# Performance work log

Hardware: AMD Instinct MI355X
Metric: run time of the kernel (lower is better)

The kernel has to match this reference:

```python
import jax, jax.numpy as jnp
import numpy as np

IC = 64   # inter_channels
S = 3     # num_subset_S
ST = 2    # num_subset_T


def _bn(x, g, b):
    # BatchNorm2d in eval mode with running_mean=0, running_var=1, eps=1e-5
    return x * (g / jnp.sqrt(1.0 + 1e-5))[:, None, None] + b[:, None, None]


def _c1(x, W, b):
    # 1x1 Conv2d over (N, C, T, V)
    return jnp.einsum('oc,nctv->notv', W, x) + b[None, :, None, None]


def setup_inputs() -> dict:
    key = jax.random.key(0)
    ks = iter(jax.random.split(key, 40))
    r = lambda sh: jax.random.normal(next(ks), sh, dtype=jnp.float32) * 0.05
    N, C, T, V = 64, 128, 64, 25
    d = {}
    d['x'] = jax.random.normal(next(ks), (N, C, T, V), dtype=jnp.float32)
    d['W_ins'] = r((2 * S * IC, C)); d['b_ins'] = r((2 * S * IC,))
    d['alphas'] = jnp.ones((1, S, 1, 1), jnp.float32)
    d['att0s'] = jnp.full((1, S, V, V), 1.0 / V, jnp.float32)
    d['W_outs'] = r((C, S * C)); d['b_outs'] = r((C,))
    d['g_outs'] = jnp.ones((C,), jnp.float32) + r((C,)); d['be_outs'] = r((C,))
    d['W_ffs'] = r((C, C)); d['b_ffs'] = r((C,))
    d['g_ffs'] = jnp.ones((C,), jnp.float32) + r((C,)); d['be_ffs'] = r((C,))
    d['W_int'] = r((4 * ST * IC, C)); d['b_int'] = r((4 * ST * IC,))
    d['alphat_b'] = jnp.ones((1, ST, 1, 1), jnp.float32)
    d['alphat_f'] = jnp.ones((1, ST, 1, 1), jnp.float32)
    d['W_outt'] = r((C, 2 * ST * C)); d['b_outt'] = r((C,))
    d['g_outt'] = jnp.ones((C,), jnp.float32) + r((C,)); d['be_outt'] = r((C,))
    d['W_fft'] = r((C, C)); d['b_fft'] = r((C,))
    d['g_fft'] = jnp.ones((C,), jnp.float32) + r((C,)); d['be_fft'] = r((C,))
    d['W_tcn'] = r((C, C, 7, 1)); d['b_tcn'] = r((C,))
    d['g_tcn'] = jnp.ones((C,), jnp.float32) + r((C,)); d['be_tcn'] = r((C,))
    return d


def reference(x, W_ins, b_ins, alphas, att0s, W_outs, b_outs, g_outs, be_outs,
              W_ffs, b_ffs, g_ffs, be_ffs, W_int, b_int, alphat_b, alphat_f,
              W_outt, b_outt, g_outt, be_outt, W_fft, b_fft, g_fft, be_fft,
              W_tcn, b_tcn, g_tcn, be_tcn):
    N, C, T, V = x.shape
    lrelu = lambda a: jax.nn.leaky_relu(a, 0.1)

    # ---- spatial attention ----
    qk = _c1(x, W_ins, b_ins).reshape(N, 2 * S, IC, T, V)
    q, k = qk[:, :S], qk[:, S:]
    att = jnp.tanh(jnp.einsum('nsctu,nsctv->nsuv', q, k) / (IC * T)) * alphas + att0s
    y = jnp.einsum('nctu,nsuv->nsctv', x, att).reshape(N, S * C, T, V)
    y = lrelu(x + _bn(_c1(y, W_outs, b_outs), g_outs, be_outs))   # out_nets + residual
    y = lrelu(x + _bn(_c1(y, W_ffs, b_ffs), g_ffs, be_ffs))       # ff_nets + residual (downs2 = identity)

    # ---- directed temporal attention ----
    bm = jnp.triu(jnp.ones((T, T), x.dtype))  # backward mask
    fm = bm.T                                  # forward mask (tril)
    qk = _c1(y, W_int, b_int).reshape(N, 4 * ST, IC, T, V)
    q_f, q_b = qk[:, :ST], qk[:, ST:2 * ST]
    k_f, k_b = qk[:, 2 * ST:3 * ST], qk[:, 3 * ST:]
    att_b = jnp.tanh(jnp.einsum('nsctv,nscqv->nstq', q_b, k_b) / (IC * V)) * alphat_b * bm
    att_f = jnp.tanh(jnp.einsum('nsctv,nscqv->nstq', q_f, k_f) / (IC * V)) * alphat_f * fm
    z_f = jnp.einsum('nctv,nstq->nscqv', y, att_f).reshape(N, ST * C, T, V)
    z_b = jnp.einsum('nctv,nstq->nscqv', y, att_b).reshape(N, ST * C, T, V)
    z = jnp.concatenate([z_f, z_b], axis=1)                        # (N, 2*ST*C, T, V)
    z = lrelu(y + _bn(_c1(z, W_outt, b_outt), g_outt, be_outt))    # out_nett + residual
    z = lrelu(y + _bn(_c1(z, W_fft, b_fft), g_fft, be_fft))        # ff_nett + residual

    # ---- TCN extension: (7,1) temporal conv + BN + residual ----
    z1 = jax.lax.conv_general_dilated(z, W_tcn, (1, 1), ((3, 3), (0, 0)),
                                      dimension_numbers=('NCHW', 'OIHW', 'NCHW'))
    z1 = _bn(z1 + b_tcn[None, :, None, None] - b_tcn[None, :, None, None] + b_tcn[None, :, None, None], g_tcn, be_tcn) if False else _bn(z1 + b_tcn[None, :, None, None], g_tcn, be_tcn)
    z = lrelu(z + z1)
    return z
```

## Files before the change

### kernel.cpp

```cpp
#include <hip/hip_runtime.h>

#define BNSC 0.99999500003749963f

typedef _Float16 f16;
typedef _Float16 f16x8 __attribute__((ext_vector_type(8)));
typedef float    f32x4 __attribute__((ext_vector_type(4)));

static __device__ __forceinline__ float lrelu_f(float a) { return a >= 0.0f ? a : 0.1f * a; }

static __device__ __forceinline__ void xcd_swz(int& bx, int& by, int& bz) {
    const int GX = gridDim.x, GY = gridDim.y, GZ = gridDim.z;
    if (((GX * GZ) & 7) == 0) {
        const int lin = blockIdx.x + GX * (blockIdx.y + GY * blockIdx.z);
        const int xcd = lin & 7;
        const int rest = lin >> 3;
        by = rest % GY;
        const int g = (rest / GY) * 8 + xcd;
        bx = g % GX;
        bz = g / GX;
    } else {
        bx = blockIdx.x; by = blockIdx.y; bz = blockIdx.z;
    }
}

__global__ __launch_bounds__(256) void prep_w_k(
    const float* __restrict__ Wins, const float* __restrict__ Wouts,
    const float* __restrict__ Wffs, const float* __restrict__ Wint,
    const float* __restrict__ Woutt, const float* __restrict__ Wfft,
    const float* __restrict__ Wtcn, f16* __restrict__ dst)
{
    int i = blockIdx.x * 256 + threadIdx.x;
    int o = 0;
    if (i < 49152) { dst[o + i] = (f16)Wins[i];  return; } i -= 49152; o += 49152;
    if (i < 49152) { dst[o + i] = (f16)Wouts[i]; return; } i -= 49152; o += 49152;
    if (i < 16384) { dst[o + i] = (f16)Wffs[i];  return; } i -= 16384; o += 16384;
    if (i < 65536) { dst[o + i] = (f16)Wint[i];  return; } i -= 65536; o += 65536;
    if (i < 65536) { dst[o + i] = (f16)Woutt[i]; return; } i -= 65536; o += 65536;
    if (i < 16384) { dst[o + i] = (f16)Wfft[i];  return; } i -= 16384; o += 16384;
    if (i < 114688) {
        int tau = i / 16384, rem = i - tau * 16384;
        dst[o + i] = (f16)Wtcn[(size_t)rem * 7 + tau];
    }
}

__global__ __launch_bounds__(256) void x_to_T_k(const float* __restrict__ x,
                                                f16* __restrict__ xT, f16* __restrict__ xBp)
{
    __shared__ float L[64 * 68];
    const int n = blockIdx.z, tv0 = blockIdx.x * 64, c0 = blockIdx.y * 64;
    const int tid = threadIdx.x;
    const int cc = tid >> 4, tv4 = (tid & 15) * 4;
    f16* xBn = xBp + (size_t)n * 262144;
    #pragma unroll
    for (int p = 0; p < 4; ++p) {
        const int c = cc + p * 16;
        float4 v = *(const float4*)&x[((size_t)n * 128 + c0 + c) * 1600 + tv0 + tv4];
        *(float4*)&L[c * 68 + tv4] = v;
        const float vv[4] = {v.x, v.y, v.z, v.w};
        #pragma unroll
        for (int e = 0; e < 4; ++e) {
            const int tvg = tv0 + tv4 + e;
            const int t = tvg / 25, u = tvg - t * 25;
            xBn[(size_t)(c0 + c) * 2048 + t * 32 + u] = (f16)vv[e];
        }
    }
    __syncthreads();
    const int tv = tid & 63, cb = (tid >> 6) * 16;
    f16x8 o0, o1;
    #pragma unroll
    for (int i = 0; i < 8; ++i) o0[i] = (f16)L[(cb + i) * 68 + tv];
    #pragma unroll
    for (int i = 0; i < 8; ++i) o1[i] = (f16)L[(cb + 8 + i) * 68 + tv];
    f16* dst = &xT[((size_t)n * 1600 + tv0 + tv) * 128 + c0 + cb];
    *(f16x8*)dst = o0;
    *(f16x8*)(dst + 8) = o1;
}

__global__ __launch_bounds__(256) void T_to_out_k(const f16* __restrict__ oT, float* __restrict__ out)
{
    __shared__ float L[128 * 69];
    const int n = blockIdx.z, tv0 = blockIdx.x * 64;
    const int tid = threadIdx.x;
    #pragma unroll
    for (int p = 0; p < 4; ++p) {
        int idx = tid + p * 256;
        int tv = idx >> 4, c8 = (idx & 15) * 8;
        f16x8 v = *(const f16x8*)&oT[((size_t)n * 1600 + tv0 + tv) * 128 + c8];
        #pragma unroll
        for (int i = 0; i < 8; ++i) L[(c8 + i) * 69 + tv] = (float)v[i];
    }
    __syncthreads();
    const int c = tid >> 1, tvb = (tid & 1) * 32;
    #pragma unroll
    for (int j = 0; j < 8; ++j) {
        float4 o;
        o.x = L[c * 69 + tvb + j * 4 + 0];
        o.y = L[c * 69 + tvb + j * 4 + 1];
        o.z = L[c * 69 + tvb + j * 4 + 2];
        o.w = L[c * 69 + tvb + j * 4 + 3];
        *(float4*)&out[((size_t)n * 128 + c) * 1600 + tv0 + tvb + j * 4] = o;
    }
}

template<int EPI>
__global__ __launch_bounds__(256) void gemm_t_k(
    const f16* __restrict__ A, const f16* __restrict__ W,
    const float* __restrict__ bias,
    const float* __restrict__ g, const float* __restrict__ be,
    const f16* __restrict__ res, f16* __restrict__ out,
    int K, int M)
{
    __shared__ __align__(16) char smem[34816];
    f16* As = (f16*)smem;
    f16* Bs = (f16*)(smem + 17408);
    float* Ss = (float*)smem;
    int bx, by, bz;
    xcd_swz(bx, by, bz);
    const int n = bz, tv0 = bx * 64, m0 = by * 64;
    const int tid = threadIdx.x;
    const int w = tid >> 6, lane = tid & 63;
    const int wr = w >> 1, wc = w & 1;
    const int lg = lane >> 4, lr = lane & 15;
    const int srow = tid >> 3;
    const int sc8 = (tid & 7) * 8;
    const f16* An = A + (size_t)n * 1600 * K;
    f32x4 acc[2][2] = {};

    for (int k0 = 0; k0 < K; k0 += 128) {
        const f16* ar0 = An + (size_t)(tv0 + srow) * K + k0;
        const f16* ar1 = An + (size_t)(tv0 + srow + 32) * K + k0;
        const f16* br0 = W + (size_t)(m0 + srow) * K + k0;
        const f16* br1 = W + (size_t)(m0 + srow + 32) * K + k0;
        uint4 a00 = *(const uint4*)(ar0 + sc8),      a01 = *(const uint4*)(ar0 + 64 + sc8);
        uint4 a10 = *(const uint4*)(ar1 + sc8),      a11 = *(const uint4*)(ar1 + 64 + sc8);
        uint4 b00 = *(const uint4*)(br0 + sc8),      b01 = *(const uint4*)(br0 + 64 + sc8);
        uint4 b10 = *(const uint4*)(br1 + sc8),      b11 = *(const uint4*)(br1 + 64 + sc8);
        __syncthreads();
        *(uint4*)&As[srow * 136 + sc8]             = a00;
        *(uint4*)&As[srow * 136 + 64 + sc8]        = a01;
        *(uint4*)&As[(srow + 32) * 136 + sc8]      = a10;
        *(uint4*)&As[(srow + 32) * 136 + 64 + sc8] = a11;
        *(uint4*)&Bs[srow * 136 + sc8]             = b00;
        *(uint4*)&Bs[srow * 136 + 64 + sc8]        = b01;
        *(uint4*)&Bs[(srow + 32) * 136 + sc8]      = b10;
        *(uint4*)&Bs[(srow + 32) * 136 + 64 + sc8] = b11;
        __syncthreads();
        #pragma unroll
        for (int kb = 0; kb < 128; kb += 32) {
            f16x8 af0 = *(const f16x8*)&As[(wr * 32 + lr) * 136 + kb + lg * 8];
            f16x8 af1 = *(const f16x8*)&As[(wr * 32 + 16 + lr) * 136 + kb + lg * 8];
            f16x8 bf0 = *(const f16x8*)&Bs[(wc * 32 + lr) * 136 + kb + lg * 8];
            f16x8 bf1 = *(const f16x8*)&Bs[(wc * 32 + 16 + lr) * 136 + kb + lg * 8];
            acc[0][0] = __builtin_amdgcn_mfma_f32_16x16x32_f16(af0, bf0, acc[0][0], 0, 0, 0);
            acc[0][1] = __builtin_amdgcn_mfma_f32_16x16x32_f16(af0, bf1, acc[0][1], 0, 0, 0);
            acc[1][0] = __builtin_amdgcn_mfma_f32_16x16x32_f16(af1, bf0, acc[1][0], 0, 0, 0);
            acc[1][1] = __builtin_amdgcn_mfma_f32_16x16x32_f16(af1, bf1, acc[1][1], 0, 0, 0);
        }
        __syncthreads();
    }
    #pragma unroll
    for (int fi = 0; fi < 2; ++fi)
        #pragma unroll
        for (int fj = 0; fj < 2; ++fj)
            #pragma unroll
            for (int rr = 0; rr < 4; ++rr)
                Ss[(wr * 32 + fi * 16 + lg * 4 + rr) * 68 + wc * 32 + fj * 16 + lr] = acc[fi][fj][rr];
    __syncthreads();
    const int tvl = tid >> 2, mq = (tid & 3) * 16;
    const int tv = tv0 + tvl;
    const int m  = m0 + mq;
    float vals[16];
    #pragma unroll
    for (int j = 0; j < 4; ++j)
        *(float4*)&vals[j * 4] = *(const float4*)&Ss[tvl * 68 + mq + j * 4];
    float bi[16];
    #pragma unroll
    for (int j = 0; j < 4; ++j) *(float4*)&bi[j * 4] = *(const float4*)&bias[m + j * 4];
    if (EPI == 1) {
        float gg[16], bb[16];
        #pragma unroll
        for (int j = 0; j < 4; ++j) {
            *(float4*)&gg[j * 4] = *(const float4*)&g[m + j * 4];
            *(float4*)&bb[j * 4] = *(const float4*)&be[m + j * 4];
        }
        const f16* rp = res + ((size_t)n * 1600 + tv) * M + m;
        f16x8 r0 = *(const f16x8*)rp;
        f16x8 r1 = *(const f16x8*)(rp + 8);
        #pragma unroll
        for (int j = 0; j < 16; ++j) {
            float r = (float)((j < 8) ? r0[j & 7] : r1[j & 7]);
            vals[j] = lrelu_f(r + (vals[j] + bi[j]) * (gg[j] * BNSC) + bb[j]);
        }
    } else {
        #pragma unroll
        for (int j = 0; j < 16; ++j) vals[j] += bi[j];
    }
    f16x8 o0, o1;
    #pragma unroll
    for (int j = 0; j < 8; ++j) { o0[j] = (f16)vals[j]; o1[j] = (f16)vals[8 + j]; }
    f16* op = out + ((size_t)n * 1600 + tv) * M + m;
    *(f16x8*)op = o0;
    *(f16x8*)(op + 8) = o1;
}

template<int K1>
__global__ __launch_bounds__(256) void fused2_k(
    const f16* __restrict__ Ain,
    const f16* __restrict__ W1,
    const float* __restrict__ b1, const float* __restrict__ g1, const float* __restrict__ be1,
    const f16* __restrict__ W2,
    const float* __restrict__ b2, const float* __restrict__ g2, const float* __restrict__ be2,
    const f16* __restrict__ res,
    f16* __restrict__ out)
{
    __shared__ __align__(16) char smem[27648];
    f16* As1  = (f16*)smem;
    f16* Bs1  = (f16*)(smem + 4608);
    float* Ss = (float*)smem;
    f16* Ys   = (f16*)smem;
    f16* Bs2  = (f16*)(smem + 8704);
    int bx, by, bz;
    xcd_swz(bx, by, bz);
    const int n = bz, tv0 = bx * 32;
    const int tid = threadIdx.x;
    const int w = tid >> 6, lane = tid & 63;
    const int wr = w >> 1, wc = w & 1;
    const int lg = lane >> 4, lr = lane & 15;
    const int srow = tid >> 3, sc = (tid & 7) * 8;
    const f16* An = Ain + (size_t)n * 1600 * K1;
    const f16* rn = res + ((size_t)n * 1600 + tv0) * 128;

    f32x4 acc[4] = {};
    for (int k0 = 0; k0 < K1; k0 += 64) {
        uint4 a0  = *(const uint4*)(An + (size_t)(tv0 + srow) * K1 + k0 + sc);
        uint4 w0  = *(const uint4*)(W1 + (size_t)srow * K1 + k0 + sc);
        uint4 w1v = *(const uint4*)(W1 + (size_t)(srow + 32) * K1 + k0 + sc);
        uint4 w2v = *(const uint4*)(W1 + (size_t)(srow + 64) * K1 + k0 + sc);
        uint4 w3v = *(const uint4*)(W1 + (size_t)(srow + 96) * K1 + k0 + sc);
        __syncthreads();
        *(uint4*)&As1[srow * 72 + sc] = a0;
        *(uint4*)&Bs1[srow * 72 + sc] = w0;
        *(uint4*)&Bs1[(srow + 32) * 72 + sc] = w1v;
        *(uint4*)&Bs1[(srow + 64) * 72 + sc] = w2v;
        *(uint4*)&Bs1[(srow + 96) * 72 + sc] = w3v;
        __syncthreads();
        #pragma unroll
        for (int kb = 0; kb < 64; kb += 32) {
            f16x8 af = *(const f16x8*)&As1[(wr * 16 + lr) * 72 + kb + lg * 8];
            #pragma unroll
            for (int ft = 0; ft < 4; ++ft) {
                f16x8 bf = *(const f16x8*)&Bs1[(wc * 64 + ft * 16 + lr) * 72 + kb + lg * 8];
                acc[ft] = __builtin_amdgcn_mfma_f32_16x16x32_f16(af, bf, acc[ft], 0, 0, 0);
            }
        }
        __syncthreads();
    }
    #pragma unroll
    for (int ft = 0; ft < 4; ++ft)
        #pragma unroll
        for (int rr = 0; rr < 4; ++rr)
            Ss[(wr * 16 + lg * 4 + rr) * 132 + wc * 64 + ft * 16 + lr] = acc[ft][rr];
    __syncthreads();
    const int tvl = tid >> 3, mq = (tid & 7) * 16;
    f16x8 yh0, yh1;
    {
        float vals[16], bb[16], gg[16], eb[16];
        #pragma unroll
        for (int j = 0; j < 4; ++j) {
            *(float4*)&vals[j * 4] = *(const float4*)&Ss[tvl * 132 + mq + j * 4];
            *(float4*)&bb[j * 4]   = *(const float4*)&b1[mq + j * 4];
            *(float4*)&gg[j * 4]   = *(const float4*)&g1[mq + j * 4];
            *(float4*)&eb[j * 4]   = *(const float4*)&be1[mq + j * 4];
        }
        const f16* rp = rn + (size_t)tvl * 128 + mq;
        f16x8 r0 = *(const f16x8*)rp, r1 = *(const f16x8*)(rp + 8);
        #pragma unroll
        for (int j = 0; j < 16; ++j) {
            float r = (float)((j < 8) ? r0[j & 7] : r1[j & 7]);
            vals[j] = lrelu_f(r + (vals[j] + bb[j]) * (gg[j] * BNSC) + eb[j]);
        }
        #pragma unroll
        for (int j = 0; j < 8; ++j) { yh0[j] = (f16)vals[j]; yh1[j] = (f16)vals[8 + j]; }
    }
    __syncthreads();
    *(f16x8*)&Ys[tvl * 136 + mq]     = yh0;
    *(f16x8*)&Ys[tvl * 136 + mq + 8] = yh1;

    f32x4 acc2[4] = {};
    for (int k2 = 0; k2 < 128; k2 += 64) {
        uint4 w0  = *(const uint4*)(W2 + (size_t)srow * 128 + k2 + sc);
        uint4 w1v = *(const uint4*)(W2 + (size_t)(srow + 32) * 128 + k2 + sc);
        uint4 w2v = *(const uint4*)(W2 + (size_t)(srow + 64) * 128 + k2 + sc);
        uint4 w3v = *(const uint4*)(W2 + (size_t)(srow + 96) * 128 + k2 + sc);
        __syncthreads();
        *(uint4*)&Bs2[srow * 72 + sc] = w0;
        *(uint4*)&Bs2[(srow + 32) * 72 + sc] = w1v;
        *(uint4*)&Bs2[(srow + 64) * 72 + sc] = w2v;
        *(uint4*)&Bs2[(srow + 96) * 72 + sc] = w3v;
        __syncthreads();
        #pragma unroll
        for (int kb = 0; kb < 64; kb += 32) {
            f16x8 af = *(const f16x8*)&Ys[(wr * 16 + lr) * 136 + k2 + kb + lg * 8];
            #pragma unroll
            for (int ft = 0; ft < 4; ++ft) {
                f16x8 bf = *(const f16x8*)&Bs2[(wc * 64 + ft * 16 + lr) * 72 + kb + lg * 8];
                acc2[ft] = __builtin_amdgcn_mfma_f32_16x16x32_f16(af, bf, acc2[ft], 0, 0, 0);
            }
        }
    }
    __syncthreads();
    #pragma unroll
    for (int ft = 0; ft < 4; ++ft)
        #pragma unroll
        for (int rr = 0; rr < 4; ++rr)
            Ss[(wr * 16 + lg * 4 + rr) * 132 + wc * 64 + ft * 16 + lr] = acc2[ft][rr];
    __syncthreads();
    {
        float vals[16], bb[16], gg[16], eb[16];
        #pragma unroll
        for (int j = 0; j < 4; ++j) {
            *(float4*)&vals[j * 4] = *(const float4*)&Ss[tvl * 132 + mq + j * 4];
            *(float4*)&bb[j * 4]   = *(const float4*)&b2[mq + j * 4];
            *(float4*)&gg[j * 4]   = *(const float4*)&g2[mq + j * 4];
            *(float4*)&eb[j * 4]   = *(const float4*)&be2[mq + j * 4];
        }
        const f16* rp = rn + (size_t)tvl * 128 + mq;
        f16x8 r0 = *(const f16x8*)rp, r1 = *(const f16x8*)(rp + 8);
        #pragma unroll
        for (int j = 0; j < 16; ++j) {
            float r = (float)((j < 8) ? r0[j & 7] : r1[j & 7]);
            vals[j] = lrelu_f(r + (vals[j] + bb[j]) * (gg[j] * BNSC) + eb[j]);
        }
        f16x8 o0, o1;
        #pragma unroll
        for (int j = 0; j < 8; ++j) { o0[j] = (f16)vals[j]; o1[j] = (f16)vals[8 + j]; }
        f16* op = out + ((size_t)n * 1600 + tv0 + tvl) * 128 + mq;
        *(f16x8*)op = o0;
        *(f16x8*)(op + 8) = o1;
    }
}

__global__ __launch_bounds__(256) void tcn_T_k(
    const f16* __restrict__ z2T, const f16* __restrict__ W7,
    const float* __restrict__ bias, const float* __restrict__ g,
    const float* __restrict__ be, f16* __restrict__ outT)
{
    __shared__ __align__(16) char smem[34816];
    f16* As = (f16*)smem;
    f16* Bs = (f16*)(smem + 17408);
    float* Ss = (float*)smem;
    int bx, by, bz;
    xcd_swz(bx, by, bz);
    const int n = bz, tv0 = bx * 64, m0 = by * 64;
    const int tid = threadIdx.x;
    const int w = tid >> 6, lane = tid & 63;
    const int wr = w >> 1, wc = w & 1;
    const int lg = lane >> 4, lr = lane & 15;
    const int srow = tid >> 3;
    const int sc8 = (tid & 7) * 8;
    const f16* Zn = z2T + (size_t)n * 204800;
    f32x4 acc[2][2] = {};

    for (int tau = 0; tau < 7; ++tau) {
        const int shift = (tau - 3) * 25;
        const f16* Wt = W7 + tau * 16384;
        const int gr0 = tv0 + srow + shift;
        const int gr1 = gr0 + 32;
        uint4 a00 = make_uint4(0,0,0,0), a01 = a00, a10 = a00, a11 = a00;
        if (gr0 >= 0 && gr0 < 1600) {
            const f16* p = Zn + (size_t)gr0 * 128;
            a00 = *(const uint4*)(p + sc8); a01 = *(const uint4*)(p + 64 + sc8);
        }
        if (gr1 >= 0 && gr1 < 1600) {
            const f16* p = Zn + (size_t)gr1 * 128;
            a10 = *(const uint4*)(p + sc8); a11 = *(const uint4*)(p + 64 + sc8);
        }
        const f16* br0 = Wt + (size_t)(m0 + srow) * 128;
        const f16* br1 = Wt + (size_t)(m0 + srow + 32) * 128;
        uint4 b00 = *(const uint4*)(br0 + sc8), b01 = *(const uint4*)(br0 + 64 + sc8);
        uint4 b10 = *(const uint4*)(br1 + sc8), b11 = *(const uint4*)(br1 + 64 + sc8);
        __syncthreads();
        *(uint4*)&As[srow * 136 + sc8]             = a00;
        *(uint4*)&As[srow * 136 + 64 + sc8]        = a01;
        *(uint4*)&As[(srow + 32) * 136 + sc8]      = a10;
        *(uint4*)&As[(srow + 32) * 136 + 64 + sc8] = a11;
        *(uint4*)&Bs[srow * 136 + sc8]             = b00;
        *(uint4*)&Bs[srow * 136 + 64 + sc8]        = b01;
        *(uint4*)&Bs[(srow + 32) * 136 + sc8]      = b10;
        *(uint4*)&Bs[(srow + 32) * 136 + 64 + sc8] = b11;
        __syncthreads();
        #pragma unroll
        for (int kb = 0; kb < 128; kb += 32) {
            f16x8 af0 = *(const f16x8*)&As[(wr * 32 + lr) * 136 + kb + lg * 8];
            f16x8 af1 = *(const f16x8*)&As[(wr * 32 + 16 + lr) * 136 + kb + lg * 8];
            f16x8 bf0 = *(const f16x8*)&Bs[(wc * 32 + lr) * 136 + kb + lg * 8];
            f16x8 bf1 = *(const f16x8*)&Bs[(wc * 32 + 16 + lr) * 136 + kb + lg * 8];
            acc[0][0] = __builtin_amdgcn_mfma_f32_16x16x32_f16(af0, bf0, acc[0][0], 0, 0, 0);
            acc[0][1] = __builtin_amdgcn_mfma_f32_16x16x32_f16(af0, bf1, acc[0][1], 0, 0, 0);
            acc[1][0] = __builtin_amdgcn_mfma_f32_16x16x32_f16(af1, bf0, acc[1][0], 0, 0, 0);
            acc[1][1] = __builtin_amdgcn_mfma_f32_16x16x32_f16(af1, bf1, acc[1][1], 0, 0, 0);
        }
        __syncthreads();
    }
    #pragma unroll
    for (int fi = 0; fi < 2; ++fi)
        #pragma unroll
        for (int fj = 0; fj < 2; ++fj)
            #pragma unroll
            for (int rr = 0; rr < 4; ++rr)
                Ss[(wr * 32 + fi * 16 + lg * 4 + rr) * 68 + wc * 32 + fj * 16 + lr] = acc[fi][fj][rr];
    __syncthreads();
    const int tvl = tid >> 2, mq = (tid & 3) * 16;
    const int tv = tv0 + tvl;
    const int m  = m0 + mq;
    float vals[16], bi[16], gg[16], bb[16];
    #pragma unroll
    for (int j = 0; j < 4; ++j) {
        *(float4*)&vals[j * 4] = *(const float4*)&Ss[tvl * 68 + mq + j * 4];
        *(float4*)&bi[j * 4]   = *(const float4*)&bias[m + j * 4];
        *(float4*)&gg[j * 4]   = *(const float4*)&g[m + j * 4];
        *(float4*)&bb[j * 4]   = *(const float4*)&be[m + j * 4];
    }
    const f16* rp = Zn + (size_t)tv * 128 + m;
    f16x8 r0 = *(const f16x8*)rp;
    f16x8 r1 = *(const f16x8*)(rp + 8);
    #pragma unroll
    for (int j = 0; j < 16; ++j) {
        float r = (float)((j < 8) ? r0[j & 7] : r1[j & 7]);
        vals[j] = lrelu_f(r + (vals[j] + bi[j]) * (gg[j] * BNSC) + bb[j]);
    }
    f16x8 o0, o1;
    #pragma unroll
    for (int j = 0; j < 8; ++j) { o0[j] = (f16)vals[j]; o1[j] = (f16)vals[8 + j]; }
    f16* op = outT + ((size_t)n * 1600 + tv) * 128 + m;
    *(f16x8*)op = o0;
    *(f16x8*)(op + 8) = o1;
}

__global__ __launch_bounds__(256) void att_s_mfma_k(
    const f16* __restrict__ QKT, float* __restrict__ P)
{
    __shared__ float Lred[4][1024];
    const int n = blockIdx.x / 24;
    const int rs = blockIdx.x % 24;
    const int s = rs >> 3, tc = rs & 7;
    const int tid = threadIdx.x;
    const int w = tid >> 6, lane = tid & 63;
    const int lg = lane >> 4, lr = lane & 15;
    const int qc = s * 64, kc = 192 + s * 64;
    const f16* Qn = QKT + (size_t)n * 1600 * 384;
    f32x4 acc[2][2] = {};

    #pragma unroll
    for (int tt = 0; tt < 2; ++tt) {
        const int t = tc * 8 + w * 2 + tt;
        const size_t rbase = (size_t)t * 25;
        #pragma unroll
        for (int kb = 0; kb < 2; ++kb) {
            f16x8 a[2] = {}, b[2] = {};
            #pragma unroll
            for (int rt = 0; rt < 2; ++rt) {
                const int u = rt * 16 + lr;
                if (u < 25) {
                    const f16* rp = Qn + (rbase + u) * 384;
                    a[rt] = *(const f16x8*)(rp + qc + kb * 32 + lg * 8);
                    b[rt] = *(const f16x8*)(rp + kc + kb * 32 + lg * 8);
                }
            }
            #pragma unroll
            for (int rt = 0; rt < 2; ++rt)
                #pragma unroll
                for (int ct = 0; ct < 2; ++ct)
                    acc[rt][ct] = __builtin_amdgcn_mfma_f32_16x16x32_f16(a[rt], b[ct], acc[rt][ct], 0, 0, 0);
        }
    }
    #pragma unroll
    for (int rt = 0; rt < 2; ++rt)
        #pragma unroll
        for (int ct = 0; ct < 2; ++ct)
            #pragma unroll
            for (int rr = 0; rr < 4; ++rr) {
                const int u = rt * 16 + lg * 4 + rr;
                const int v = ct * 16 + lr;
                Lred[w][u * 32 + v] = acc[rt][ct][rr];
            }
    __syncthreads();
    float* Pp = P + (((size_t)n * 3 + s) * 8 + tc) * 1024;
    for (int i = tid; i < 1024; i += 256)
        Pp[i] = Lred[0][i] + Lred[1][i] + Lred[2][i] + Lred[3][i];
}

__global__ __launch_bounds__(256) void att_s_fin_k(
    const float* __restrict__ P, const float* __restrict__ alphas,
    const float* __restrict__ att0s, float* __restrict__ att)
{
    const int n = blockIdx.x / 3, s = blockIdx.x % 3;
    const float* Pp = P + ((size_t)n * 3 + s) * 8192;
    const float al = alphas[s];
    for (int p = threadIdx.x; p < 625; p += 256) {
        const int u = p / 25, v = p - u * 25;
        float sum = 0.f;
        #pragma unroll
        for (int tc = 0; tc < 8; ++tc) sum += Pp[tc * 1024 + u * 32 + v];
        att[((size_t)n * 3 + s) * 625 + p] = tanhf(sum * (1.0f / 4096.0f)) * al + att0s[s * 625 + p];
    }
}

__global__ __launch_bounds__(256) void att_t_mfma_k(
    const f16* __restrict__ QKT,
    const float* __restrict__ alphat_b, const float* __restrict__ alphat_f,
    float* __restrict__ att)
{
    __shared__ f16 Qs[64 * 72];
    __shared__ f16 Ks[64 * 72];
    const int n = blockIdx.x >> 2, r = blockIdx.x & 3;
    const int br = r >> 1, s = r & 1;
    const int qg = ((br == 0) ? s : 2 + s) * 64;
    const int kg = ((br == 0) ? 4 + s : 6 + s) * 64;
    const f16* Qn = QKT + (size_t)n * 1600 * 512;
    const int tid = threadIdx.x;
    const int w = tid >> 6, lane = tid & 63;
    const int lg = lane >> 4, lr = lane & 15;
    const int srow = tid >> 2, scol = (tid & 3) * 16;
    f32x4 acc[4] = {};

    for (int v = 0; v < 25; ++v) {
        const f16* rowp = Qn + (size_t)(srow * 25 + v) * 512;
        uint4 q0 = *(const uint4*)(rowp + qg + scol);
        uint4 q1 = *(const uint4*)(rowp + qg + scol + 8);
        uint4 k0 = *(const uint4*)(rowp + kg + scol);
        uint4 k1 = *(const uint4*)(rowp + kg + scol + 8);
        __syncthreads();
        *(uint4*)&Qs[srow * 72 + scol] = q0;
        *(uint4*)&Qs[srow * 72 + scol + 8] = q1;
        *(uint4*)&Ks[srow * 72 + scol] = k0;
        *(uint4*)&Ks[srow * 72 + scol + 8] = k1;
        __syncthreads();
        #pragma unroll
        for (int kb = 0; kb < 2; ++kb) {
            f16x8 a = *(const f16x8*)&Qs[(w * 16 + lr) * 72 + kb * 32 + lg * 8];
            #pragma unroll
            for (int ct = 0; ct < 4; ++ct) {
                f16x8 b = *(const f16x8*)&Ks[(ct * 16 + lr) * 72 + kb * 32 + lg * 8];
                acc[ct] = __builtin_amdgcn_mfma_f32_16x16x32_f16(a, b, acc[ct], 0, 0, 0);
            }
        }
    }
    const float al = (br == 0) ? alphat_f[s] : alphat_b[s];
    float* ap = att + (((size_t)n * 2 + br) * 2 + s) * 4096;
    #pragma unroll
    for (int ct = 0; ct < 4; ++ct) {
        #pragma unroll
        for (int rr = 0; rr < 4; ++rr) {
            const int t = w * 16 + lg * 4 + rr;
            const int q = ct * 16 + lr;
            const bool keep = (br == 0) ? (t >= q) : (q >= t);
            ap[t * 64 + q] = keep ? tanhf(acc[ct][rr] * (1.0f / 1600.0f)) * al : 0.0f;
        }
    }
}

__global__ __launch_bounds__(256) void apply_s_mfma_k(
    const f16* __restrict__ xBp, const float* __restrict__ att, f16* __restrict__ y1T)
{
    __shared__ f16 As[3 * 32 * 48];
    const int n = blockIdx.x >> 6, t = blockIdx.x & 63;
    const int tid = threadIdx.x;
    const int w = tid >> 6, lane = tid & 63;
    const int lg = lane >> 4, lr = lane & 15;
    const float* an = att + (size_t)n * 1875;
    for (int i = tid; i < 3 * 32 * 48; i += 256) {
        int s = i / 1536, r2 = i - s * 1536;
        int v = r2 / 48, u = r2 - v * 48;
        As[i] = (v < 25 && u < 25) ? (f16)an[s * 625 + u * 25 + v] : (f16)0.f;
    }
    __syncthreads();
    const f16* Bn = xBp + (size_t)n * 262144 + (size_t)t * 32;
    f16x8 bf[2];
    #pragma unroll
    for (int ct = 0; ct < 2; ++ct)
        bf[ct] = *(const f16x8*)(Bn + (size_t)(w * 32 + ct * 16 + lr) * 2048 + lg * 8);
    #pragma unroll
    for (int s = 0; s < 3; ++s) {
        f32x4 acc[2][2] = {};
        #pragma unroll
        for (int vt = 0; vt < 2; ++vt) {
            f16x8 a = *(const f16x8*)&As[s * 1536 + (vt * 16 + lr) * 48 + lg * 8];
            #pragma unroll
            for (int ct = 0; ct < 2; ++ct)
                acc[vt][ct] = __builtin_amdgcn_mfma_f32_16x16x32_f16(a, bf[ct], acc[vt][ct], 0, 0, 0);
        }
        #pragma unroll
        for (int vt = 0; vt < 2; ++vt)
            #pragma unroll
            for (int ct = 0; ct < 2; ++ct)
                #pragma unroll
                for (int rr = 0; rr < 4; ++rr) {
                    const int v = vt * 16 + lg * 4 + rr;
                    if (v < 25) {
                        const int c = w * 32 + ct * 16 + lr;
                        y1T[((size_t)n * 1600 + t * 25 + v) * 384 + s * 128 + c] = (f16)acc[vt][ct][rr];
                    }
                }
    }
}

__global__ __launch_bounds__(256) void t_to_B_k(
    const f16* __restrict__ y2T, f16* __restrict__ Y2B)
{
    __shared__ f16 L[64 * 136];
    const int n = blockIdx.x, v = blockIdx.y;
    const f16* Yn = y2T + (size_t)n * 204800;
    const int tid = threadIdx.x;
    for (int i = tid; i < 1024; i += 256) {
        int t = i >> 4, c8 = (i & 15) * 8;
        *(f16x8*)&L[t * 136 + c8] = *(const f16x8*)&Yn[(size_t)(t * 25 + v) * 128 + c8];
    }
    __syncthreads();
    const int c = tid >> 1, t0 = (tid & 1) * 32;
    f16* dst = Y2B + ((size_t)n * 25 + v) * 8192 + (size_t)c * 64 + t0;
    #pragma unroll
    for (int j = 0; j < 4; ++j) {
        f16x8 o;
        #pragma unroll
        for (int e = 0; e < 8; ++e) o[e] = L[(t0 + j * 8 + e) * 136 + c];
        *(f16x8*)(dst + j * 8) = o;
    }
}

__global__ __launch_bounds__(256) void apply_t_mfma_k(
    const f16* __restrict__ Y2B, const float* __restrict__ att, f16* __restrict__ zT)
{
    __shared__ f16 AsT[4][64 * 72];
    const int n = blockIdx.x;
    const int by = blockIdx.y;
    const int vg = by >> 1;
    const int ch = (by & 1) * 64;
    const int tid = threadIdx.x;
    const int w = tid >> 6, lane = tid & 63;
    const int lg = lane >> 4, lr = lane & 15;
    const float* ap = att + (size_t)n * 4 * 4096;
    for (int i = tid; i < 4 * 4096; i += 256) {
        int r = i >> 12, rem = i & 4095;
        int t = rem >> 6, q = rem & 63;
        AsT[r][q * 72 + t] = (f16)ap[i];
    }
    __syncthreads();
    f16x8 af[4][2];
    #pragma unroll
    for (int qt = 0; qt < 4; ++qt)
        #pragma unroll
        for (int kb = 0; kb < 2; ++kb)
            af[qt][kb] = *(const f16x8*)&AsT[w][(qt * 16 + lr) * 72 + kb * 32 + lg * 8];

    for (int vi = 0; vi < 5; ++vi) {
        const int v = vg * 5 + vi;
        const f16* Bv = Y2B + ((size_t)n * 25 + v) * 8192 + (size_t)ch * 64;
        f32x4 acc[4][4] = {};
        #pragma unroll
        for (int kb = 0; kb < 2; ++kb)
            #pragma unroll
            for (int ct = 0; ct < 4; ++ct) {
                f16x8 bf = *(const f16x8*)(Bv + (size_t)(ct * 16 + lr) * 64 + kb * 32 + lg * 8);
                #pragma unroll
                for (int qt = 0; qt < 4; ++qt)
                    acc[qt][ct] = __builtin_amdgcn_mfma_f32_16x16x32_f16(af[qt][kb], bf, acc[qt][ct], 0, 0, 0);
            }
        #pragma unroll
        for (int qt = 0; qt < 4; ++qt)
            #pragma unroll
            for (int ct = 0; ct < 4; ++ct)
                #pragma unroll
                for (int rr = 0; rr < 4; ++rr) {
                    const int q = qt * 16 + lg * 4 + rr;
                    const int c = ch + ct * 16 + lr;
                    zT[((size_t)n * 1600 + q * 25 + v) * 512 + w * 128 + c] = (f16)acc[qt][ct][rr];
                }
    }
}

extern "C" void kernel_launch(void* const* d_in, const int* in_sizes, int n_in,
                              void* d_out, int out_size, void* d_ws, size_t ws_size,
                              hipStream_t stream) {
    const float* x       = (const float*)d_in[0];
    const float* W_ins   = (const float*)d_in[1];
    const float* b_ins   = (const float*)d_in[2];
    const float* alphas  = (const float*)d_in[3];
    const float* att0s   = (const float*)d_in[4];
    const float* W_outs  = (const float*)d_in[5];
    const float* b_outs  = (const float*)d_in[6];
    const float* g_outs  = (const float*)d_in[7];
    const float* be_outs = (const float*)d_in[8];
    const float* W_ffs   = (const float*)d_in[9];
    const float* b_ffs   = (const float*)d_in[10];
    const float* g_ffs   = (const float*)d_in[11];
    const float* be_ffs  = (const float*)d_in[12];
    const float* W_int   = (const float*)d_in[13];
    const float* b_int   = (const float*)d_in[14];
    const float* alphat_b= (const float*)d_in[15];
    const float* alphat_f= (const float*)d_in[16];
    const float* W_outt  = (const float*)d_in[17];
    const float* b_outt  = (const float*)d_in[18];
    const float* g_outt  = (const float*)d_in[19];
    const float* be_outt = (const float*)d_in[20];
    const float* W_fft   = (const float*)d_in[21];
    const float* b_fft   = (const float*)d_in[22];
    const float* g_fft   = (const float*)d_in[23];
    const float* be_fft  = (const float*)d_in[24];
    const float* W_tcn   = (const float*)d_in[25];
    const float* b_tcn   = (const float*)d_in[26];
    const float* g_tcn   = (const float*)d_in[27];
    const float* be_tcn  = (const float*)d_in[28];

    f16* wf = (f16*)d_ws;
    f16* W_ins16  = wf;
    f16* W_outs16 = wf + 49152;
    f16* W_ffs16  = wf + 98304;
    f16* W_int16  = wf + 114688;
    f16* W_outt16 = wf + 180224;
    f16* W_fft16  = wf + 245760;
    f16* W_tcn16  = wf + 262144;
    const size_t wbytes = 753664;

    const size_t perN = (819200ull + 3ull * 204800ull + 204800ull + 262144ull) * 2ull;
    int Nc = 64;
    while (Nc > 4 && wbytes + (size_t)Nc * perN > ws_size) Nc >>= 1;

    f16* A   = (f16*)((char*)d_ws + wbytes);
    f16* B   = A   + (size_t)Nc * 819200;
    f16* C   = B   + (size_t)Nc * 204800;
    f16* D   = C   + (size_t)Nc * 204800;
    f16* Y2B = D   + (size_t)Nc * 204800;
    f16* xBp = Y2B + (size_t)Nc * 204800;
    float* P    = (float*)Y2B;
    float* attS = (float*)Y2B + (size_t)Nc * 24576;
    float* attT = (float*)B;

    prep_w_k<<<1472, 256, 0, stream>>>(W_ins, W_outs, W_ffs, W_int, W_outt, W_fft, W_tcn, wf);

    for (int n0 = 0; n0 < 64; n0 += Nc) {
        const float* xc = x + (size_t)n0 * 204800;
        float* outc     = (float*)d_out + (size_t)n0 * 204800;

        x_to_T_k<<<dim3(25, 2, Nc), 256, 0, stream>>>(xc, D, xBp);
        gemm_t_k<0><<<dim3(25, 6, Nc), 256, 0, stream>>>(D, W_ins16, b_ins, nullptr, nullptr,
                                                         nullptr, A, 128, 384);
        att_s_mfma_k<<<dim3(24 * Nc), 256, 0, stream>>>(A, P);
        att_s_fin_k<<<dim3(3 * Nc), 256, 0, stream>>>(P, alphas, att0s, attS);
        apply_s_mfma_k<<<dim3(64 * Nc), 256, 0, stream>>>(xBp, attS, A);
        fused2_k<384><<<dim3(50, 1, Nc), 256, 0, stream>>>(A, W_outs16, b_outs, g_outs, be_outs,
                                                           W_ffs16, b_ffs, g_ffs, be_ffs, D, C);
        t_to_B_k<<<dim3(Nc, 25), 256, 0, stream>>>(C, Y2B);
        gemm_t_k<0><<<dim3(25, 8, Nc), 256, 0, stream>>>(C, W_int16, b_int, nullptr, nullptr,
                                                         nullptr, A, 128, 512);
        att_t_mfma_k<<<dim3(4 * Nc), 256, 0, stream>>>(A, alphat_b, alphat_f, attT);
        apply_t_mfma_k<<<dim3(Nc, 10), 256, 0, stream>>>(Y2B, attT, A);
        fused2_k<512><<<dim3(50, 1, Nc), 256, 0, stream>>>(A, W_outt16, b_outt, g_outt, be_outt,
                                                           W_fft16, b_fft, g_fft, be_fft, C, D);
        tcn_T_k<<<dim3(25, 2, Nc), 256, 0, stream>>>(D, W_tcn16, b_tcn, g_tcn, be_tcn, A);
        T_to_out_k<<<dim3(25, 1, Nc), 256, 0, stream>>>(A, outc);
    }
}
```

Baseline: 414.6 us.

## Enlarge fused2 tile to 64 rows with 512 threads and 2x2 MFMA warp tiles

The fused double-GEMM kernel now processes 64 tv rows per block with 8 waves arranged 2x4, each computing a 32x32 output via 2x2 MFMA fragments. The weight tiles loaded per block are shared across twice as many rows, halving weight traffic per output and improving fragment reuse in registers. The cost is half as many blocks, larger shared memory per block, and potentially lower occupancy.

```diff
diff --git a/kernel.cpp b/kernel.cpp
--- a/kernel.cpp
+++ b/kernel.cpp
@@ -204,7 +204,7 @@
 }
 
 template<int K1>
-__global__ __launch_bounds__(256) void fused2_k(
+__global__ __launch_bounds__(512) void fused2_k(
     const f16* __restrict__ Ain,
     const f16* __restrict__ W1,
     const float* __restrict__ b1, const float* __restrict__ g1, const float* __restrict__ be1,
@@ -213,53 +213,53 @@
     const f16* __restrict__ res,
     f16* __restrict__ out)
 {
-    __shared__ __align__(16) char smem[27648];
+    __shared__ __align__(16) char smem[35840];
     f16* As1  = (f16*)smem;
-    f16* Bs1  = (f16*)(smem + 4608);
+    f16* Bs1  = (f16*)(smem + 9216);
     float* Ss = (float*)smem;
     f16* Ys   = (f16*)smem;
-    f16* Bs2  = (f16*)(smem + 8704);
+    f16* Bs2  = (f16*)(smem + 17408);
     int bx, by, bz;
     xcd_swz(bx, by, bz);
-    const int n = bz, tv0 = bx * 32;
+    const int n = bz, tv0 = bx * 64;
     const int tid = threadIdx.x;
     const int w = tid >> 6, lane = tid & 63;
-    const int wr = w >> 1, wc = w & 1;
+    const int wr = w >> 2, wc = w & 3;
     const int lg = lane >> 4, lr = lane & 15;
     const int srow = tid >> 3, sc = (tid & 7) * 8;
     const f16* An = Ain + (size_t)n * 1600 * K1;
     const f16* rn = res + ((size_t)n * 1600 + tv0) * 128;
 
-    f32x4 acc[4] = {};
+    f32x4 acc[2][2] = {};
     for (int k0 = 0; k0 < K1; k0 += 64) {
         uint4 a0  = *(const uint4*)(An + (size_t)(tv0 + srow) * K1 + k0 + sc);
         uint4 w0  = *(const uint4*)(W1 + (size_t)srow * K1 + k0 + sc);
-        uint4 w1v = *(const uint4*)(W1 + (size_t)(srow + 32) * K1 + k0 + sc);
-        uint4 w2v = *(const uint4*)(W1 + (size_t)(srow + 64) * K1 + k0 + sc);
-        uint4 w3v = *(const uint4*)(W1 + (size_t)(srow + 96) * K1 + k0 + sc);
+        uint4 w1v = *(const uint4*)(W1 + (size_t)(srow + 64) * K1 + k0 + sc);
         __syncthreads();
         *(uint4*)&As1[srow * 72 + sc] = a0;
         *(uint4*)&Bs1[srow * 72 + sc] = w0;
-        *(uint4*)&Bs1[(srow + 32) * 72 + sc] = w1v;
-        *(uint4*)&Bs1[(srow + 64) * 72 + sc] = w2v;
-        *(uint4*)&Bs1[(srow + 96) * 72 + sc] = w3v;
+        *(uint4*)&Bs1[(srow + 64) * 72 + sc] = w1v;
         __syncthreads();
         #pragma unroll
         for (int kb = 0; kb < 64; kb += 32) {
-            f16x8 af = *(const f16x8*)&As1[(wr * 16 + lr) * 72 + kb + lg * 8];
-            #pragma unroll
-            for (int ft = 0; ft < 4; ++ft) {
-                f16x8 bf = *(const f16x8*)&Bs1[(wc * 64 + ft * 16 + lr) * 72 + kb + lg * 8];
-                acc[ft] = __builtin_amdgcn_mfma_f32_16x16x32_f16(af, bf, acc[ft], 0, 0, 0);
-            }
-        }
-        __syncthreads();
-    }
-    #pragma unroll
-    for (int ft = 0; ft < 4; ++ft)
-        #pragma unroll
-        for (int rr = 0; rr < 4; ++rr)
-            Ss[(wr * 16 + lg * 4 + rr) * 132 + wc * 64 + ft * 16 + lr] = acc[ft][rr];
+            f16x8 af0 = *(const f16x8*)&As1[(wr * 32 + lr) * 72 + kb + lg * 8];
+            f16x8 af1 = *(const f16x8*)&As1[(wr * 32 + 16 + lr) * 72 + kb + lg * 8];
+            f16x8 bf0 = *(const f16x8*)&Bs1[(wc * 32 + lr) * 72 + kb + lg * 8];
+            f16x8 bf1 = *(const f16x8*)&Bs1[(wc * 32 + 16 + lr) * 72 + kb + lg * 8];
+            acc[0][0] = __builtin_amdgcn_mfma_f32_16x16x32_f16(af0, bf0, acc[0][0], 0, 0, 0);
+            acc[0][1] = __builtin_amdgcn_mfma_f32_16x16x32_f16(af0, bf1, acc[0][1], 0, 0, 0);
+            acc[1][0] = __builtin_amdgcn_mfma_f32_16x16x32_f16(af1, bf0, acc[1][0], 0, 0, 0);
+            acc[1][1] = __builtin_amdgcn_mfma_f32_16x16x32_f16(af1, bf1, acc[1][1], 0, 0, 0);
+        }
+        __syncthreads();
+    }
+    #pragma unroll
+    for (int fi = 0; fi < 2; ++fi)
+        #pragma unroll
+        for (int fj = 0; fj < 2; ++fj)
+            #pragma unroll
+            for (int rr = 0; rr < 4; ++rr)
+                Ss[(wr * 32 + fi * 16 + lg * 4 + rr) * 132 + wc * 32 + fj * 16 + lr] = acc[fi][fj][rr];
     __syncthreads();
     const int tvl = tid >> 3, mq = (tid & 7) * 16;
     f16x8 yh0, yh1;
@@ -286,34 +286,34 @@
     *(f16x8*)&Ys[tvl * 136 + mq]     = yh0;
     *(f16x8*)&Ys[tvl * 136 + mq + 8] = yh1;
 
-    f32x4 acc2[4] = {};
+    f32x4 acc2[2][2] = {};
     for (int k2 = 0; k2 < 128; k2 += 64) {
         uint4 w0  = *(const uint4*)(W2 + (size_t)srow * 128 + k2 + sc);
-        uint4 w1v = *(const uint4*)(W2 + (size_t)(srow + 32) * 128 + k2 + sc);
-        uint4 w2v = *(const uint4*)(W2 + (size_t)(srow + 64) * 128 + k2 + sc);
-        uint4 w3v = *(const uint4*)(W2 + (size_t)(srow + 96) * 128 + k2 + sc);
+        uint4 w1v = *(const uint4*)(W2 + (size_t)(srow + 64) * 128 + k2 + sc);
         __syncthreads();
         *(uint4*)&Bs2[srow * 72 + sc] = w0;
-        *(uint4*)&Bs2[(srow + 32) * 72 + sc] = w1v;
-        *(uint4*)&Bs2[(srow + 64) * 72 + sc] = w2v;
-        *(uint4*)&Bs2[(srow + 96) * 72 + sc] = w3v;
+        *(uint4*)&Bs2[(srow + 64) * 72 + sc] = w1v;
         __syncthreads();
         #pragma unroll
         for (int kb = 0; kb < 64; kb += 32) {
-            f16x8 af = *(const f16x8*)&Ys[(wr * 16 + lr) * 136 + k2 + kb + lg * 8];
-            #pragma unroll
-            for (int ft = 0; ft < 4; ++ft) {
-                f16x8 bf = *(const f16x8*)&Bs2[(wc * 64 + ft * 16 + lr) * 72 + kb + lg * 8];
-                acc2[ft] = __builtin_amdgcn_mfma_f32_16x16x32_f16(af, bf, acc2[ft], 0, 0, 0);
-            }
-        }
-    }
-    __syncthreads();
-    #pragma unroll
-    for (int ft = 0; ft < 4; ++ft)
-        #pragma unroll
-        for (int rr = 0; rr < 4; ++rr)
-            Ss[(wr * 16 + lg * 4 + rr) * 132 + wc * 64 + ft * 16 + lr] = acc2[ft][rr];
+            f16x8 af0 = *(const f16x8*)&Ys[(wr * 32 + lr) * 136 + k2 + kb + lg * 8];
+            f16x8 af1 = *(const f16x8*)&Ys[(wr * 32 + 16 + lr) * 136 + k2 + kb + lg * 8];
+            f16x8 bf0 = *(const f16x8*)&Bs2[(wc * 32 + lr) * 72 + kb + lg * 8];
+            f16x8 bf1 = *(const f16x8*)&Bs2[(wc * 32 + 16 + lr) * 72 + kb + lg * 8];
+            acc2[0][0] = __builtin_amdgcn_mfma_f32_16x16x32_f16(af0, bf0, acc2[0][0], 0, 0, 0);
+            acc2[0][1] = __builtin_amdgcn_mfma_f32_16x16x32_f16(af0, bf1, acc2[0][1], 0, 0, 0);
+            acc2[1][0] = __builtin_amdgcn_mfma_f32_16x16x32_f16(af1, bf0, acc2[1][0], 0, 0, 0);
+            acc2[1][1] = __builtin_amdgcn_mfma_f32_16x16x32_f16(af1, bf1, acc2[1][1], 0, 0, 0);
+        }
+        __syncthreads();
+    }
+    #pragma unroll
+    for (int fi = 0; fi < 2; ++fi)
+        #pragma unroll
+        for (int fj = 0; fj < 2; ++fj)
+            #pragma unroll
+            for (int rr = 0; rr < 4; ++rr)
+                Ss[(wr * 32 + fi * 16 + lg * 4 + rr) * 132 + wc * 32 + fj * 16 + lr] = acc2[fi][fj][rr];
     __syncthreads();
     {
         float vals[16], bb[16], gg[16], eb[16];
@@ -748,14 +748,14 @@
         att_s_mfma_k<<<dim3(24 * Nc), 256, 0, stream>>>(A, P);
         att_s_fin_k<<<dim3(3 * Nc), 256, 0, stream>>>(P, alphas, att0s, attS);
         apply_s_mfma_k<<<dim3(64 * Nc), 256, 0, stream>>>(xBp, attS, A);
-        fused2_k<384><<<dim3(50, 1, Nc), 256, 0, stream>>>(A, W_outs16, b_outs, g_outs, be_outs,
+        fused2_k<384><<<dim3(25, 1, Nc), 512, 0, stream>>>(A, W_outs16, b_outs, g_outs, be_outs,
                                                            W_ffs16, b_ffs, g_ffs, be_ffs, D, C);
         t_to_B_k<<<dim3(Nc, 25), 256, 0, stream>>>(C, Y2B);
         gemm_t_k<0><<<dim3(25, 8, Nc), 256, 0, stream>>>(C, W_int16, b_int, nullptr, nullptr,
                                                          nullptr, A, 128, 512);
         att_t_mfma_k<<<dim3(4 * Nc), 256, 0, stream>>>(A, alphat_b, alphat_f, attT);
         apply_t_mfma_k<<<dim3(Nc, 10), 256, 0, stream>>>(Y2B, attT, A);
-        fused2_k<512><<<dim3(50, 1, Nc), 256, 0, stream>>>(A, W_outt16, b_outt, g_outt, be_outt,
+        fused2_k<512><<<dim3(25, 1, Nc), 512, 0, stream>>>(A, W_outt16, b_outt, g_outt, be_outt,
                                                            W_fft16, b_fft, g_fft, be_fft, C, D);
         tcn_T_k<<<dim3(25, 2, Nc), 256, 0, stream>>>(D, W_tcn16, b_tcn, g_tcn, be_tcn, A);
         T_to_out_k<<<dim3(25, 1, Nc), 256, 0, stream>>>(A, outc);
```

New measurement: 415.4 us. About the same (+0.2%).
